# Kernel optimization log

Hardware: AMD Instinct MI355X
Metric: run time of the kernel (lower is better)

## Reference

```python
import jax, jax.numpy as jnp
import numpy as np

MIN_NORM = 1e-15
PROJ_EPS = 4e-3   # HGCN fp32 boundary eps
C = 1.0           # curvature (args.c)
SQRT_C = 1.0
LOOP_ATT = 10.0   # self-loop weight


def _norm(x):
    return jnp.clip(jnp.linalg.norm(x, axis=-1, keepdims=True), MIN_NORM)


def artanh(x):
    x = jnp.clip(x, -1.0 + 1e-6, 1.0 - 1e-6)
    return 0.5 * (jnp.log1p(x) - jnp.log1p(-x))


def proj(x):
    # project back inside the Poincare ball
    n = _norm(x)
    maxn = (1.0 - PROJ_EPS) / SQRT_C
    return jnp.where(n > maxn, x / n * maxn, x)


def expmap0(u):
    n = _norm(u)
    return jnp.tanh(SQRT_C * n) * u / (SQRT_C * n)


def logmap0(p):
    n = _norm(p)
    return artanh(SQRT_C * n) * p / (SQRT_C * n)


def mobius_add(x, y):
    x2 = jnp.sum(x * x, -1, keepdims=True)
    y2 = jnp.sum(y * y, -1, keepdims=True)
    xy = jnp.sum(x * y, -1, keepdims=True)
    num = (1.0 + 2.0 * C * xy + C * y2) * x + (1.0 - C * x2) * y
    den = 1.0 + 2.0 * C * xy + C * C * x2 * y2
    return num / jnp.clip(den, MIN_NORM)


def mobius_matvec(W, x):
    xn = _norm(x)
    mx = x @ W.T                       # [N, out]
    mxn = _norm(mx)
    res = jnp.tanh(mxn / xn * artanh(SQRT_C * xn)) * mx / (mxn * SQRT_C)
    zero = jnp.all(mx == 0, axis=-1, keepdims=True)
    return jnp.where(zero, 0.0, res)


def normalize_adj(adj):
    # symmetric D^{-1/2} A D^{-1/2}
    deg = jnp.sum(adj, axis=-1)
    dinv = jnp.where(deg > 0, deg ** -0.5, 0.0)
    return dinv[:, None] * adj * dinv[None, :]


def encode(x, adj, W_stack, b_stack):
    # map features onto the manifold: proj(expmap0(proj_tan0(x))) ; proj_tan0 = id
    h = proj(expmap0(x))
    for i in range(W_stack.shape[0]):
        # HypLinear: mobius matvec + hyperbolic bias add
        m = proj(mobius_matvec(W_stack[i], h))
        hb = proj(expmap0(b_stack[i][None, :]))
        m = proj(mobius_add(m, hb))
        # HypAgg: aggregate in tangent space at origin
        m = proj(expmap0(adj @ logmap0(m)))
        # HypAct: relu in tangent space
        h = proj(expmap0(jax.nn.relu(logmap0(m))))
    return h


def readout(h):
    # cat(global_avg_pool, global_max_pool) over nodes -> [2*d]
    return jnp.concatenate([jnp.mean(h, axis=0), jnp.max(h, axis=0)])


def setup_inputs() -> dict:
    key = jax.random.key(0)
    ks = jax.random.split(key, 12)
    N, F, D, L = 4096, 128, 128, 2
    x1 = jax.random.normal(ks[0], (1, N, F), jnp.float32)
    x2 = jax.random.normal(ks[1], (1, N, F), jnp.float32)
    adj1 = jax.random.uniform(ks[2], (1, N, N), dtype=jnp.float32)
    adj2 = jax.random.uniform(ks[3], (1, N, N), dtype=jnp.float32)
    dist1 = jax.random.uniform(ks[4], (N, N), dtype=jnp.float32)
    dist2 = jax.random.uniform(ks[5], (N, N), dtype=jnp.float32)
    W_stack = jax.random.normal(ks[6], (L, D, F), jnp.float32) * 0.05
    b_stack = jax.random.normal(ks[7], (L, D), jnp.float32) * 0.01
    W_mlp1 = jax.random.normal(ks[8], (D, 6 * D), jnp.float32) * 0.05
    b_mlp1 = jnp.zeros((D,), jnp.float32)
    W_mlp2 = jax.random.normal(ks[9], (1, D), jnp.float32) * 0.05
    b_mlp2 = jnp.zeros((1,), jnp.float32)
    return dict(x1=x1, x2=x2, adj1=adj1, adj2=adj2, dist1=dist1, dist2=dist2,
                W_stack=W_stack, b_stack=b_stack,
                W_mlp1=W_mlp1, b_mlp1=b_mlp1, W_mlp2=W_mlp2, b_mlp2=b_mlp2)


def reference(x1, x2, adj1, adj2, dist1, dist2, W_stack, b_stack,
              W_mlp1, b_mlp1, W_mlp2, b_mlp2):
    N = x1.shape[1]
    eye = jnp.eye(N, dtype=x1.dtype)
    a1 = normalize_adj(adj1[0] + LOOP_ATT * eye)
    a2 = normalize_adj(adj2[0] + LOOP_ATT * eye)
    out1 = encode(x1[0], a1, W_stack, b_stack)
    out2 = encode(x2[0], a2, W_stack, b_stack)
    h1 = readout(out1)
    h2 = readout(out2)
    feat = jnp.concatenate([h1, h2, h1 - h2])            # [6*d]
    hidden = jax.nn.gelu(feat @ W_mlp1.T + b_mlp1, approximate=False)
    logits = hidden @ W_mlp2.T + b_mlp2                  # [1]
    return logits
```

## Files before the change

kernel.cpp:

```cpp
#include <hip/hip_runtime.h>
#include <math.h>

#define MIN_NORM 1e-15f
#define MAXN 0.996f

typedef __attribute__((ext_vector_type(8))) short bf16x8;
typedef __attribute__((ext_vector_type(16))) float f32x16;

union U8 { unsigned short s[8]; bf16x8 v; };

static __device__ __forceinline__ float wsum(float v) {
#pragma unroll
    for (int o = 32; o > 0; o >>= 1) v += __shfl_xor(v, o, 64);
    return v;
}
static __device__ __forceinline__ float artanh_f(float x) {
    const float lim = 1.0f - 1e-6f;
    x = fminf(fmaxf(x, -lim), lim);
    return 0.5f * (log1pf(x) - log1pf(-x));
}

static __device__ __forceinline__ void split3(float a, unsigned short& h,
                                              unsigned short& l, unsigned short& ll) {
    unsigned u = __float_as_uint(a);
    unsigned hb = u & 0xFFFF0000u;
    float r1 = a - __uint_as_float(hb);
    unsigned u1 = __float_as_uint(r1);
    unsigned lb = u1 & 0xFFFF0000u;
    float r2 = r1 - __uint_as_float(lb);
    unsigned u2 = __float_as_uint(r2);
    unsigned t = u2 + 0x7FFFu + ((u2 >> 16) & 1u);
    h = (unsigned short)(hb >> 16);
    l = (unsigned short)(lb >> 16);
    ll = (unsigned short)(t >> 16);
}

__global__ void k_transW(const float* __restrict__ W, float* __restrict__ Wt) {
    int l = blockIdx.y;
    int t = blockIdx.x * 256 + threadIdx.x;
    int k = t >> 7, d = t & 127;
    Wt[l * 16384 + k * 128 + d] = W[l * 16384 + d * 128 + k];
}

__global__ void k_hb(const float* __restrict__ b_stack, float* __restrict__ hb) {
    int l = blockIdx.x;
    int lane = threadIdx.x;
    float2 b = ((const float2*)(b_stack + l * 128))[lane];
    float n = fmaxf(sqrtf(wsum(b.x * b.x + b.y * b.y)), MIN_NORM);
    float sc = tanhf(n) / n;
    float hx = sc * b.x, hy = sc * b.y;
    float nm = fmaxf(sqrtf(wsum(hx * hx + hy * hy)), MIN_NORM);
    if (nm > MAXN) { float s = MAXN / nm; hx *= s; hy *= s; }
    ((float2*)(hb + l * 128))[lane] = make_float2(hx, hy);
}

__global__ __launch_bounds__(256) void k_deg(const float* __restrict__ adj1,
                                             const float* __restrict__ adj2,
                                             float* __restrict__ dinv) {
    int row = blockIdx.x, g = blockIdx.y;
    const float* adj = (g ? adj2 : adj1) + (size_t)row * 4096;
    float s = 0.f;
    for (int i = threadIdx.x; i < 1024; i += 256) {
        float4 v = ((const float4*)adj)[i];
        s += v.x + v.y + v.z + v.w;
    }
    s = wsum(s);
    __shared__ float ls[4];
    if ((threadIdx.x & 63) == 0) ls[threadIdx.x >> 6] = s;
    __syncthreads();
    if (threadIdx.x == 0) {
        float t = ls[0] + ls[1] + ls[2] + ls[3] + 10.0f;
        dinv[g * 4096 + row] = (t > 0.f) ? (1.0f / sqrtf(t)) : 0.f;
    }
}

__global__ __launch_bounds__(256) void k_manifold(const float* __restrict__ x1,
                                                  const float* __restrict__ x2,
                                                  float* __restrict__ h) {
    int wid = threadIdx.x >> 6, lane = threadIdx.x & 63;
    int row = blockIdx.x * 4 + wid;
    const float* x = (row < 4096 ? x1 : x2 - (size_t)4096 * 128) + (size_t)row * 128;
    float2 v = ((const float2*)x)[lane];
    float n = fmaxf(sqrtf(wsum(v.x * v.x + v.y * v.y)), MIN_NORM);
    float sc = tanhf(n) / n;
    float hx = sc * v.x, hy = sc * v.y;
    float nm = fmaxf(sqrtf(wsum(hx * hx + hy * hy)), MIN_NORM);
    if (nm > MAXN) { float s = MAXN / nm; hx *= s; hy *= s; }
    ((float2*)(h + (size_t)row * 128))[lane] = make_float2(hx, hy);
}

__global__ __launch_bounds__(256) void k_lin(const float* __restrict__ A,
                                             const float* __restrict__ Bt,
                                             float* __restrict__ C) {
    int r0 = blockIdx.x * 64;
    __shared__ float As[32][64];
    __shared__ float Bs[32][128];
    int t = threadIdx.x;
    int tx = t & 15, ty = t >> 4;
    float acc[4][8] = {};
    int ar = t >> 3;
    int ac = (t & 7) * 4;
    for (int kt = 0; kt < 128; kt += 32) {
        const float* Ap = A + (size_t)(r0 + ar) * 128 + kt + ac;
        float4 v0 = *(const float4*)Ap;
        float4 v1 = *(const float4*)(Ap + 32 * 128);
        As[ac + 0][ar] = v0.x; As[ac + 1][ar] = v0.y; As[ac + 2][ar] = v0.z; As[ac + 3][ar] = v0.w;
        As[ac + 0][ar + 32] = v1.x; As[ac + 1][ar + 32] = v1.y; As[ac + 2][ar + 32] = v1.z; As[ac + 3][ar + 32] = v1.w;
#pragma unroll
        for (int i = 0; i < 4; i++) {
            int f = t + 256 * i;
            int kr = f >> 5, c = (f & 31) * 4;
            *(float4*)&Bs[kr][c] = *(const float4*)(Bt + (size_t)(kt + kr) * 128 + c);
        }
        __syncthreads();
#pragma unroll
        for (int k = 0; k < 32; k++) {
            float4 a = *(const float4*)&As[k][ty * 4];
            float4 b0 = *(const float4*)&Bs[k][tx * 4];
            float4 b1 = *(const float4*)&Bs[k][64 + tx * 4];
            float av[4] = {a.x, a.y, a.z, a.w};
            float bv[8] = {b0.x, b0.y, b0.z, b0.w, b1.x, b1.y, b1.z, b1.w};
#pragma unroll
            for (int i = 0; i < 4; i++)
#pragma unroll
                for (int j = 0; j < 8; j++)
                    acc[i][j] = fmaf(av[i], bv[j], acc[i][j]);
        }
        __syncthreads();
    }
#pragma unroll
    for (int i = 0; i < 4; i++) {
        float* Cr = C + (size_t)(r0 + ty * 4 + i) * 128;
        *(float4*)(Cr + tx * 4) = make_float4(acc[i][0], acc[i][1], acc[i][2], acc[i][3]);
        *(float4*)(Cr + 64 + tx * 4) = make_float4(acc[i][4], acc[i][5], acc[i][6], acc[i][7]);
    }
}

__global__ __launch_bounds__(256) void k_postlin(const float* __restrict__ h,
                                                 const float* __restrict__ mx,
                                                 const float* __restrict__ hb,
                                                 const float* __restrict__ dinv,
                                                 float* __restrict__ tp) {
    int wid = threadIdx.x >> 6, lane = threadIdx.x & 63;
    int row = blockIdx.x * 4 + wid;
    float2 hv = ((const float2*)(h + (size_t)row * 128))[lane];
    float2 mv = ((const float2*)(mx + (size_t)row * 128))[lane];
    float xn = fmaxf(sqrtf(wsum(hv.x * hv.x + hv.y * hv.y)), MIN_NORM);
    float mxn = fmaxf(sqrtf(wsum(mv.x * mv.x + mv.y * mv.y)), MIN_NORM);
    float arg = mxn / xn * artanh_f(xn);
    float sc = tanhf(arg) / mxn;
    float rx = sc * mv.x, ry = sc * mv.y;
    float nr = fmaxf(sqrtf(wsum(rx * rx + ry * ry)), MIN_NORM);
    if (nr > MAXN) { float s = MAXN / nr; rx *= s; ry *= s; }
    float2 bv = ((const float2*)hb)[lane];
    float x2 = wsum(rx * rx + ry * ry);
    float y2 = wsum(bv.x * bv.x + bv.y * bv.y);
    float xy = wsum(rx * bv.x + ry * bv.y);
    float cx = 1.0f + 2.0f * xy + y2;
    float cy = 1.0f - x2;
    float den = fmaxf(1.0f + 2.0f * xy + x2 * y2, MIN_NORM);
    float mxo = (cx * rx + cy * bv.x) / den;
    float myo = (cx * ry + cy * bv.y) / den;
    float nm = fmaxf(sqrtf(wsum(mxo * mxo + myo * myo)), MIN_NORM);
    if (nm > MAXN) { float s = MAXN / nm; mxo *= s; myo *= s; }
    float nm2 = fmaxf(sqrtf(wsum(mxo * mxo + myo * myo)), MIN_NORM);
    float lsc = artanh_f(nm2) / nm2;
    float dv = dinv[row];
    ((float2*)(tp + (size_t)row * 128))[lane] =
        make_float2(dv * (lsc * mxo), dv * (lsc * myo));
}

__global__ __launch_bounds__(256) void k_tsplit(const float* __restrict__ tp,
                                                unsigned short* __restrict__ Ph,
                                                unsigned short* __restrict__ Pl,
                                                unsigned short* __restrict__ Pll) {
    __shared__ float L[64][128];
    int g = blockIdx.y;
    int k0 = blockIdx.x * 64;
    const float* T = tp + ((size_t)g * 4096 + k0) * 128;
    int t = threadIdx.x;
#pragma unroll
    for (int i = 0; i < 8; i++) {
        int f = t + 256 * i;
        int r = f >> 5, c4 = f & 31;
        *(float4*)&L[r][c4 * 4] = *(const float4*)(T + (size_t)r * 128 + c4 * 4);
    }
    __syncthreads();
    int c = t & 127, lhi = t >> 7;
    int c31 = c & 31, ct = c >> 5;
#pragma unroll
    for (int q = 0; q < 4; q++) {
        int kb = (k0 >> 4) + q;
        U8 ah, al, al2;
#pragma unroll
        for (int j = 0; j < 8; j++)
            split3(L[q * 16 + lhi * 8 + j][c], ah.s[j], al.s[j], al2.s[j]);
        size_t off = ((((size_t)g * 256 + kb) * 4 + ct) * 64 + lhi * 32 + c31) * 8;
        *(bf16x8*)(Ph + off) = ah.v;
        *(bf16x8*)(Pl + off) = al.v;
        *(bf16x8*)(Pll + off) = al2.v;
    }
}

__global__ __launch_bounds__(256, 2) void k_agg_mfma(
    const float* __restrict__ adj1, const float* __restrict__ adj2,
    const unsigned short* __restrict__ Ph, const unsigned short* __restrict__ Pl,
    const unsigned short* __restrict__ Pll, float* __restrict__ part) {
    __shared__ __align__(16) unsigned short Bs[2][12][512];
    const int w = threadIdx.x >> 6, lane = threadIdx.x & 63;
    const int mt = blockIdx.x, ks = blockIdx.y, g = blockIdx.z;
    const float* __restrict__ A = g ? adj2 : adj1;
    const int l31 = lane & 31, lhi = lane >> 5;
    const float* Ap = A + (size_t)(mt * 128 + w * 32 + l31) * 4096 + ks * 512 + lhi * 8;

    const unsigned short* src[3];
#pragma unroll
    for (int i = 0; i < 3; i++) {
        int c = w * 3 + i;
        const unsigned short* Pb = (c < 4) ? Ph : ((c < 8) ? Pl : Pll);
        src[i] = Pb + ((((size_t)(g * 256 + ks * 32)) * 4 + (c & 3)) * 64 + lane) * 8;
    }

    f32x16 acc[4] = {};
    float4 a0 = *(const float4*)Ap, a1 = *(const float4*)(Ap + 4);

    {
        bf16x8 r0 = *(const bf16x8*)(src[0]);
        bf16x8 r1 = *(const bf16x8*)(src[1]);
        bf16x8 r2 = *(const bf16x8*)(src[2]);
        *(bf16x8*)&Bs[0][w * 3 + 0][lane * 8] = r0;
        *(bf16x8*)&Bs[0][w * 3 + 1][lane * 8] = r1;
        *(bf16x8*)&Bs[0][w * 3 + 2][lane * 8] = r2;
    }
    __syncthreads();

    for (int t = 0; t < 32; t++) {
        const int cur = t & 1;
        const bool more = (t + 1 < 32);
        bf16x8 r0, r1, r2;
        if (more) {
            size_t adv = (size_t)(t + 1) * 2048;
            r0 = *(const bf16x8*)(src[0] + adv);
            r1 = *(const bf16x8*)(src[1] + adv);
            r2 = *(const bf16x8*)(src[2] + adv);
        }
        const float* An = more ? (Ap + 16) : Ap;
        float4 n0 = *(const float4*)An;
        float4 n1 = *(const float4*)(An + 4);
        Ap += 16;
        bf16x8 bh[4], bl[4], bll[4];
#pragma unroll
        for (int ct = 0; ct < 4; ct++) {
            bh[ct]  = *(const bf16x8*)&Bs[cur][ct][lane * 8];
            bl[ct]  = *(const bf16x8*)&Bs[cur][4 + ct][lane * 8];
            bll[ct] = *(const bf16x8*)&Bs[cur][8 + ct][lane * 8];
        }
        U8 ah, al, al2;
        float av[8] = {a0.x, a0.y, a0.z, a0.w, a1.x, a1.y, a1.z, a1.w};
#pragma unroll
        for (int j = 0; j < 8; j++) split3(av[j], ah.s[j], al.s[j], al2.s[j]);
#pragma unroll
        for (int ct = 0; ct < 4; ct++)
            acc[ct] = __builtin_amdgcn_mfma_f32_32x32x16_bf16(ah.v, bh[ct], acc[ct], 0, 0, 0);
#pragma unroll
        for (int ct = 0; ct < 4; ct++)
            acc[ct] = __builtin_amdgcn_mfma_f32_32x32x16_bf16(al.v, bh[ct], acc[ct], 0, 0, 0);
#pragma unroll
        for (int ct = 0; ct < 4; ct++)
            acc[ct] = __builtin_amdgcn_mfma_f32_32x32x16_bf16(ah.v, bl[ct], acc[ct], 0, 0, 0);
#pragma unroll
        for (int ct = 0; ct < 4; ct++)
            acc[ct] = __builtin_amdgcn_mfma_f32_32x32x16_bf16(al.v, bl[ct], acc[ct], 0, 0, 0);
#pragma unroll
        for (int ct = 0; ct < 4; ct++)
            acc[ct] = __builtin_amdgcn_mfma_f32_32x32x16_bf16(ah.v, bll[ct], acc[ct], 0, 0, 0);
#pragma unroll
        for (int ct = 0; ct < 4; ct++)
            acc[ct] = __builtin_amdgcn_mfma_f32_32x32x16_bf16(al2.v, bh[ct], acc[ct], 0, 0, 0);
        if (more) {
            const int nb = cur ^ 1;
            *(bf16x8*)&Bs[nb][w * 3 + 0][lane * 8] = r0;
            *(bf16x8*)&Bs[nb][w * 3 + 1][lane * 8] = r1;
            *(bf16x8*)&Bs[nb][w * 3 + 2][lane * 8] = r2;
        }
        asm volatile("s_waitcnt lgkmcnt(0)" ::: "memory");
        __builtin_amdgcn_sched_barrier(0);
        __builtin_amdgcn_s_barrier();
        a0 = n0; a1 = n1;
    }

    float* P = part + ((size_t)(g * 8 + ks) * 4096) * 128;
    const int rb = mt * 128 + w * 32 + 4 * lhi;
#pragma unroll
    for (int ct = 0; ct < 4; ct++) {
        const int c = ct * 32 + l31;
#pragma unroll
        for (int q = 0; q < 16; q++) {
            int r = rb + (q & 3) + 8 * (q >> 2);
            P[(size_t)r * 128 + c] = acc[ct][q];
        }
    }
}

__global__ __launch_bounds__(256) void k_reduce(const float* __restrict__ part,
                                                const float* __restrict__ tp,
                                                const float* __restrict__ dinv,
                                                float* __restrict__ h) {
    int wid = threadIdx.x >> 6, lane = threadIdx.x & 63;
    int row = blockIdx.x * 4 + wid;
    int g = row >> 12, rr = row & 4095;
    float sx = 0.f, sy = 0.f;
    const float* P = part + ((size_t)(g * 8) * 4096 + rr) * 128;
#pragma unroll
    for (int ks = 0; ks < 8; ks++) {
        float2 v = ((const float2*)(P + (size_t)ks * 4096 * 128))[lane];
        sx += v.x; sy += v.y;
    }
    float2 tv = ((const float2*)(tp + (size_t)row * 128))[lane];
    float d = dinv[row];
    float vx = d * (sx + 10.0f * tv.x);
    float vy = d * (sy + 10.0f * tv.y);
    float n = fmaxf(sqrtf(wsum(vx * vx + vy * vy)), MIN_NORM);
    float e = tanhf(n) / n;
    float px = e * vx, py = e * vy;
    float nm = fmaxf(sqrtf(wsum(px * px + py * py)), MIN_NORM);
    if (nm > MAXN) { float s = MAXN / nm; px *= s; py *= s; }
    float nm2 = fmaxf(sqrtf(wsum(px * px + py * py)), MIN_NORM);
    float lsc = artanh_f(nm2) / nm2;
    float tx2 = fmaxf(lsc * px, 0.0f), ty2 = fmaxf(lsc * py, 0.0f);
    float nr = fmaxf(sqrtf(wsum(tx2 * tx2 + ty2 * ty2)), MIN_NORM);
    float e2 = tanhf(nr) / nr;
    float hx = e2 * tx2, hy = e2 * ty2;
    float nh = fmaxf(sqrtf(wsum(hx * hx + hy * hy)), MIN_NORM);
    if (nh > MAXN) { float s = MAXN / nh; hx *= s; hy *= s; }
    ((float2*)(h + (size_t)row * 128))[lane] = make_float2(hx, hy);
}

__global__ __launch_bounds__(256) void k_red_part(const float* __restrict__ h,
                                                  float* __restrict__ part) {
    int chunk = blockIdx.x;
    int col = threadIdx.x & 127, half = threadIdx.x >> 7;
    float s = 0.f, m = -INFINITY;
    for (int i = 0; i < 64; i++) {
        int r = chunk * 128 + half * 64 + i;
        float v = h[(size_t)r * 128 + col];
        s += v;
        m = fmaxf(m, v);
    }
    __shared__ float ss[128], sm[128];
    if (half) { ss[col] = s; sm[col] = m; }
    __syncthreads();
    if (!half) {
        s += ss[col];
        m = fmaxf(m, sm[col]);
        part[(chunk * 2 + 0) * 128 + col] = s;
        part[(chunk * 2 + 1) * 128 + col] = m;
    }
}

__global__ void k_red_final(const float* __restrict__ part, float* __restrict__ feat) {
    int g = blockIdx.x, col = threadIdx.x;
    float s = 0.f, m = -INFINITY;
    for (int c = g * 32; c < g * 32 + 32; c++) {
        s += part[(c * 2 + 0) * 128 + col];
        m = fmaxf(m, part[(c * 2 + 1) * 128 + col]);
    }
    feat[g * 256 + col] = s * (1.0f / 4096.0f);
    feat[g * 256 + 128 + col] = m;
}

__global__ __launch_bounds__(256) void k_mlp_hidden(const float* __restrict__ feat,
                                                    const float* __restrict__ W1,
                                                    const float* __restrict__ b1,
                                                    float* __restrict__ hidden) {
    int j = blockIdx.x;
    int t = threadIdx.x;
    float p = 0.f;
    for (int k = t; k < 768; k += 256) {
        float f = (k < 512) ? feat[k] : (feat[k - 512] - feat[k - 256]);
        p = fmaf(f, W1[j * 768 + k], p);
    }
    p = wsum(p);
    __shared__ float ps[4];
    if ((t & 63) == 0) ps[t >> 6] = p;
    __syncthreads();
    if (t == 0) {
        float x = ps[0] + ps[1] + ps[2] + ps[3] + b1[j];
        hidden[j] = 0.5f * x * (1.0f + erff(x * 0.70710678118654752f));
    }
}

__global__ void k_mlp_out(const float* __restrict__ hidden, const float* __restrict__ W2,
                          const float* __restrict__ b2, float* __restrict__ out) {
    int t = threadIdx.x;
    float v = hidden[t] * W2[t];
    v = wsum(v);
    __shared__ float ps[2];
    if ((t & 63) == 0) ps[t >> 6] = v;
    __syncthreads();
    if (t == 0) out[0] = ps[0] + ps[1] + b2[0];
}

extern "C" void kernel_launch(void* const* d_in, const int* in_sizes, int n_in,
                              void* d_out, int out_size, void* d_ws, size_t ws_size,
                              hipStream_t stream) {
    (void)in_sizes; (void)n_in; (void)out_size; (void)ws_size;
    const float* x1 = (const float*)d_in[0];
    const float* x2 = (const float*)d_in[1];
    const float* adj1 = (const float*)d_in[2];
    const float* adj2 = (const float*)d_in[3];
    const float* W_stack = (const float*)d_in[6];
    const float* b_stack = (const float*)d_in[7];
    const float* W1 = (const float*)d_in[8];
    const float* b1 = (const float*)d_in[9];
    const float* W2 = (const float*)d_in[10];
    const float* b2 = (const float*)d_in[11];

    float* ws = (float*)d_ws;
    float* dinv = ws;
    float* hb   = ws + 8192;
    float* Wt   = ws + 8448;
    float* h    = ws + 41216;
    float* mx   = h + 1048576;
    float* tp   = mx + 1048576;
    float* part = tp + 1048576;
    float* rpart = part + 8388608;
    float* feat = rpart + 16384;
    float* hid  = feat + 512;
    unsigned short* Ph  = (unsigned short*)(hid + 128);
    unsigned short* Pl  = Ph + 2 * 128 * 4096;
    unsigned short* Pll = Pl + 2 * 128 * 4096;

    k_transW<<<dim3(64, 2), 256, 0, stream>>>(W_stack, Wt);
    k_hb<<<2, 64, 0, stream>>>(b_stack, hb);
    k_deg<<<dim3(4096, 2), 256, 0, stream>>>(adj1, adj2, dinv);
    k_manifold<<<2048, 256, 0, stream>>>(x1, x2, h);
    for (int l = 0; l < 2; l++) {
        k_lin<<<128, 256, 0, stream>>>(h, Wt + l * 16384, mx);
        k_postlin<<<2048, 256, 0, stream>>>(h, mx, hb + l * 128, dinv, tp);
        k_tsplit<<<dim3(64, 2), 256, 0, stream>>>(tp, Ph, Pl, Pll);
        k_agg_mfma<<<dim3(32, 8, 2), 256, 0, stream>>>(adj1, adj2, Ph, Pl, Pll, part);
        k_reduce<<<2048, 256, 0, stream>>>(part, tp, dinv, h);
    }
    k_red_part<<<64, 256, 0, stream>>>(h, rpart);
    k_red_final<<<2, 128, 0, stream>>>(rpart, feat);
    k_mlp_hidden<<<128, 256, 0, stream>>>(feat, W1, b1, hid);
    k_mlp_out<<<1, 128, 0, stream>>>(hid, W2, b2, (float*)d_out);
}
```

Before: 218.1 us.

## Fuse small kernels and double K-step per barrier in MFMA aggregation

Merges the W transpose with the bias expmap kernel, fuses the post-linear manifold math into the bf16 split kernel, and folds the readout finalisation and both MLP layers into one single-block tail kernel. This cuts kernel launches and drops one tp round-trip through global memory. The aggregation MFMA loop now handles two 16-wide K chunks per iteration with a larger LDS buffer, halving barrier count. The fused post-lin kernel launches only 128 blocks instead of 2048, which lowers parallelism for that stage, and the larger LDS footprint may reduce occupancy.

```diff
diff --git a/kernel.cpp b/kernel.cpp
--- a/kernel.cpp
+++ b/kernel.cpp
@@ -35,23 +35,22 @@
     ll = (unsigned short)(t >> 16);
 }
 
-__global__ void k_transW(const float* __restrict__ W, float* __restrict__ Wt) {
+__global__ void k_transW_hb(const float* __restrict__ W, float* __restrict__ Wt,
+                            const float* __restrict__ b_stack, float* __restrict__ hb) {
     int l = blockIdx.y;
     int t = blockIdx.x * 256 + threadIdx.x;
     int k = t >> 7, d = t & 127;
     Wt[l * 16384 + k * 128 + d] = W[l * 16384 + d * 128 + k];
-}
-
-__global__ void k_hb(const float* __restrict__ b_stack, float* __restrict__ hb) {
-    int l = blockIdx.x;
-    int lane = threadIdx.x;
-    float2 b = ((const float2*)(b_stack + l * 128))[lane];
-    float n = fmaxf(sqrtf(wsum(b.x * b.x + b.y * b.y)), MIN_NORM);
-    float sc = tanhf(n) / n;
-    float hx = sc * b.x, hy = sc * b.y;
-    float nm = fmaxf(sqrtf(wsum(hx * hx + hy * hy)), MIN_NORM);
-    if (nm > MAXN) { float s = MAXN / nm; hx *= s; hy *= s; }
-    ((float2*)(hb + l * 128))[lane] = make_float2(hx, hy);
+    if (blockIdx.x == 0 && threadIdx.x < 64) {
+        int lane = threadIdx.x;
+        float2 b = ((const float2*)(b_stack + l * 128))[lane];
+        float n = fmaxf(sqrtf(wsum(b.x * b.x + b.y * b.y)), MIN_NORM);
+        float sc = tanhf(n) / n;
+        float hx = sc * b.x, hy = sc * b.y;
+        float nm = fmaxf(sqrtf(wsum(hx * hx + hy * hy)), MIN_NORM);
+        if (nm > MAXN) { float s = MAXN / nm; hx *= s; hy *= s; }
+        ((float2*)(hb + l * 128))[lane] = make_float2(hx, hy);
+    }
 }
 
 __global__ __launch_bounds__(256) void k_deg(const float* __restrict__ adj1,
@@ -136,56 +135,51 @@
     }
 }
 
-__global__ __launch_bounds__(256) void k_postlin(const float* __restrict__ h,
-                                                 const float* __restrict__ mx,
-                                                 const float* __restrict__ hb,
-                                                 const float* __restrict__ dinv,
-                                                 float* __restrict__ tp) {
-    int wid = threadIdx.x >> 6, lane = threadIdx.x & 63;
-    int row = blockIdx.x * 4 + wid;
-    float2 hv = ((const float2*)(h + (size_t)row * 128))[lane];
-    float2 mv = ((const float2*)(mx + (size_t)row * 128))[lane];
-    float xn = fmaxf(sqrtf(wsum(hv.x * hv.x + hv.y * hv.y)), MIN_NORM);
-    float mxn = fmaxf(sqrtf(wsum(mv.x * mv.x + mv.y * mv.y)), MIN_NORM);
-    float arg = mxn / xn * artanh_f(xn);
-    float sc = tanhf(arg) / mxn;
-    float rx = sc * mv.x, ry = sc * mv.y;
-    float nr = fmaxf(sqrtf(wsum(rx * rx + ry * ry)), MIN_NORM);
-    if (nr > MAXN) { float s = MAXN / nr; rx *= s; ry *= s; }
-    float2 bv = ((const float2*)hb)[lane];
-    float x2 = wsum(rx * rx + ry * ry);
-    float y2 = wsum(bv.x * bv.x + bv.y * bv.y);
-    float xy = wsum(rx * bv.x + ry * bv.y);
-    float cx = 1.0f + 2.0f * xy + y2;
-    float cy = 1.0f - x2;
-    float den = fmaxf(1.0f + 2.0f * xy + x2 * y2, MIN_NORM);
-    float mxo = (cx * rx + cy * bv.x) / den;
-    float myo = (cx * ry + cy * bv.y) / den;
-    float nm = fmaxf(sqrtf(wsum(mxo * mxo + myo * myo)), MIN_NORM);
-    if (nm > MAXN) { float s = MAXN / nm; mxo *= s; myo *= s; }
-    float nm2 = fmaxf(sqrtf(wsum(mxo * mxo + myo * myo)), MIN_NORM);
-    float lsc = artanh_f(nm2) / nm2;
-    float dv = dinv[row];
-    ((float2*)(tp + (size_t)row * 128))[lane] =
-        make_float2(dv * (lsc * mxo), dv * (lsc * myo));
-}
-
-__global__ __launch_bounds__(256) void k_tsplit(const float* __restrict__ tp,
-                                                unsigned short* __restrict__ Ph,
-                                                unsigned short* __restrict__ Pl,
-                                                unsigned short* __restrict__ Pll) {
+__global__ __launch_bounds__(256) void k_posttsplit(const float* __restrict__ h,
+                                                    const float* __restrict__ mx,
+                                                    const float* __restrict__ hb,
+                                                    const float* __restrict__ dinv,
+                                                    float* __restrict__ tp,
+                                                    unsigned short* __restrict__ Ph,
+                                                    unsigned short* __restrict__ Pl,
+                                                    unsigned short* __restrict__ Pll) {
     __shared__ float L[64][128];
     int g = blockIdx.y;
     int k0 = blockIdx.x * 64;
-    const float* T = tp + ((size_t)g * 4096 + k0) * 128;
+    int w = threadIdx.x >> 6, lane = threadIdx.x & 63;
+    for (int q = 0; q < 16; q++) {
+        int r = w * 16 + q;
+        int row = g * 4096 + k0 + r;
+        float2 hv = ((const float2*)(h + (size_t)row * 128))[lane];
+        float2 mv = ((const float2*)(mx + (size_t)row * 128))[lane];
+        float xn = fmaxf(sqrtf(wsum(hv.x * hv.x + hv.y * hv.y)), MIN_NORM);
+        float mxn = fmaxf(sqrtf(wsum(mv.x * mv.x + mv.y * mv.y)), MIN_NORM);
+        float arg = mxn / xn * artanh_f(xn);
+        float sc = tanhf(arg) / mxn;
+        float rx = sc * mv.x, ry = sc * mv.y;
+        float nr = fmaxf(sqrtf(wsum(rx * rx + ry * ry)), MIN_NORM);
+        if (nr > MAXN) { float s = MAXN / nr; rx *= s; ry *= s; }
+        float2 bv = ((const float2*)hb)[lane];
+        float x2 = wsum(rx * rx + ry * ry);
+        float y2 = wsum(bv.x * bv.x + bv.y * bv.y);
+        float xy = wsum(rx * bv.x + ry * bv.y);
+        float cx = 1.0f + 2.0f * xy + y2;
+        float cy = 1.0f - x2;
+        float den = fmaxf(1.0f + 2.0f * xy + x2 * y2, MIN_NORM);
+        float mxo = (cx * rx + cy * bv.x) / den;
+        float myo = (cx * ry + cy * bv.y) / den;
+        float nm = fmaxf(sqrtf(wsum(mxo * mxo + myo * myo)), MIN_NORM);
+        if (nm > MAXN) { float s = MAXN / nm; mxo *= s; myo *= s; }
+        float nm2 = fmaxf(sqrtf(wsum(mxo * mxo + myo * myo)), MIN_NORM);
+        float lsc = artanh_f(nm2) / nm2;
+        float dv = dinv[row];
+        float ox = dv * (lsc * mxo), oy = dv * (lsc * myo);
+        L[r][2 * lane] = ox;
+        L[r][2 * lane + 1] = oy;
+        ((float2*)(tp + (size_t)row * 128))[lane] = make_float2(ox, oy);
+    }
+    __syncthreads();
     int t = threadIdx.x;
-#pragma unroll
-    for (int i = 0; i < 8; i++) {
-        int f = t + 256 * i;
-        int r = f >> 5, c4 = f & 31;
-        *(float4*)&L[r][c4 * 4] = *(const float4*)(T + (size_t)r * 128 + c4 * 4);
-    }
-    __syncthreads();
     int c = t & 127, lhi = t >> 7;
     int c31 = c & 31, ct = c >> 5;
 #pragma unroll
@@ -202,11 +196,45 @@
     }
 }
 
+static __device__ __forceinline__ void step16(const unsigned short Bsc[][512], int cb,
+                                              int lane, float4 a0, float4 a1,
+                                              f32x16* acc) {
+    bf16x8 bh[4], bl[4], bll[4];
+#pragma unroll
+    for (int ct = 0; ct < 4; ct++) {
+        bh[ct]  = *(const bf16x8*)&Bsc[cb + ct][lane * 8];
+        bl[ct]  = *(const bf16x8*)&Bsc[cb + 4 + ct][lane * 8];
+        bll[ct] = *(const bf16x8*)&Bsc[cb + 8 + ct][lane * 8];
+    }
+    U8 ah, al, al2;
+    float av[8] = {a0.x, a0.y, a0.z, a0.w, a1.x, a1.y, a1.z, a1.w};
+#pragma unroll
+    for (int j = 0; j < 8; j++) split3(av[j], ah.s[j], al.s[j], al2.s[j]);
+#pragma unroll
+    for (int ct = 0; ct < 4; ct++)
+        acc[ct] = __builtin_amdgcn_mfma_f32_32x32x16_bf16(ah.v, bh[ct], acc[ct], 0, 0, 0);
+#pragma unroll
+    for (int ct = 0; ct < 4; ct++)
+        acc[ct] = __builtin_amdgcn_mfma_f32_32x32x16_bf16(al.v, bh[ct], acc[ct], 0, 0, 0);
+#pragma unroll
+    for (int ct = 0; ct < 4; ct++)
+        acc[ct] = __builtin_amdgcn_mfma_f32_32x32x16_bf16(ah.v, bl[ct], acc[ct], 0, 0, 0);
+#pragma unroll
+    for (int ct = 0; ct < 4; ct++)
+        acc[ct] = __builtin_amdgcn_mfma_f32_32x32x16_bf16(al.v, bl[ct], acc[ct], 0, 0, 0);
+#pragma unroll
+    for (int ct = 0; ct < 4; ct++)
+        acc[ct] = __builtin_amdgcn_mfma_f32_32x32x16_bf16(ah.v, bll[ct], acc[ct], 0, 0, 0);
+#pragma unroll
+    for (int ct = 0; ct < 4; ct++)
+        acc[ct] = __builtin_amdgcn_mfma_f32_32x32x16_bf16(al2.v, bh[ct], acc[ct], 0, 0, 0);
+}
+
 __global__ __launch_bounds__(256, 2) void k_agg_mfma(
     const float* __restrict__ adj1, const float* __restrict__ adj2,
     const unsigned short* __restrict__ Ph, const unsigned short* __restrict__ Pl,
     const unsigned short* __restrict__ Pll, float* __restrict__ part) {
-    __shared__ __align__(16) unsigned short Bs[2][12][512];
+    __shared__ __align__(16) unsigned short Bs[2][24][512];
     const int w = threadIdx.x >> 6, lane = threadIdx.x & 63;
     const int mt = blockIdx.x, ks = blockIdx.y, g = blockIdx.z;
     const float* __restrict__ A = g ? adj2 : adj1;
@@ -222,71 +250,57 @@
     }
 
     f32x16 acc[4] = {};
-    float4 a0 = *(const float4*)Ap, a1 = *(const float4*)(Ap + 4);
+    float4 a0 = *(const float4*)Ap,        a1 = *(const float4*)(Ap + 4);
+    float4 a2 = *(const float4*)(Ap + 16), a3 = *(const float4*)(Ap + 20);
 
     {
         bf16x8 r0 = *(const bf16x8*)(src[0]);
         bf16x8 r1 = *(const bf16x8*)(src[1]);
         bf16x8 r2 = *(const bf16x8*)(src[2]);
+        bf16x8 r3 = *(const bf16x8*)(src[0] + 2048);
+        bf16x8 r4 = *(const bf16x8*)(src[1] + 2048);
+        bf16x8 r5 = *(const bf16x8*)(src[2] + 2048);
         *(bf16x8*)&Bs[0][w * 3 + 0][lane * 8] = r0;
         *(bf16x8*)&Bs[0][w * 3 + 1][lane * 8] = r1;
         *(bf16x8*)&Bs[0][w * 3 + 2][lane * 8] = r2;
-    }
-    __syncthreads();
-
-    for (int t = 0; t < 32; t++) {
-        const int cur = t & 1;
-        const bool more = (t + 1 < 32);
-        bf16x8 r0, r1, r2;
+        *(bf16x8*)&Bs[0][12 + w * 3 + 0][lane * 8] = r3;
+        *(bf16x8*)&Bs[0][12 + w * 3 + 1][lane * 8] = r4;
+        *(bf16x8*)&Bs[0][12 + w * 3 + 2][lane * 8] = r5;
+    }
+    __syncthreads();
+
+    for (int p = 0; p < 16; p++) {
+        const int cur = p & 1;
+        const bool more = (p + 1 < 16);
+        bf16x8 r0, r1, r2, r3, r4, r5;
         if (more) {
-            size_t adv = (size_t)(t + 1) * 2048;
+            size_t adv = (size_t)(2 * (p + 1)) * 2048;
             r0 = *(const bf16x8*)(src[0] + adv);
             r1 = *(const bf16x8*)(src[1] + adv);
             r2 = *(const bf16x8*)(src[2] + adv);
-        }
-        const float* An = more ? (Ap + 16) : Ap;
-        float4 n0 = *(const float4*)An;
-        float4 n1 = *(const float4*)(An + 4);
-        Ap += 16;
-        bf16x8 bh[4], bl[4], bll[4];
-#pragma unroll
-        for (int ct = 0; ct < 4; ct++) {
-            bh[ct]  = *(const bf16x8*)&Bs[cur][ct][lane * 8];
-            bl[ct]  = *(const bf16x8*)&Bs[cur][4 + ct][lane * 8];
-            bll[ct] = *(const bf16x8*)&Bs[cur][8 + ct][lane * 8];
-        }
-        U8 ah, al, al2;
-        float av[8] = {a0.x, a0.y, a0.z, a0.w, a1.x, a1.y, a1.z, a1.w};
-#pragma unroll
-        for (int j = 0; j < 8; j++) split3(av[j], ah.s[j], al.s[j], al2.s[j]);
-#pragma unroll
-        for (int ct = 0; ct < 4; ct++)
-            acc[ct] = __builtin_amdgcn_mfma_f32_32x32x16_bf16(ah.v, bh[ct], acc[ct], 0, 0, 0);
-#pragma unroll
-        for (int ct = 0; ct < 4; ct++)
-            acc[ct] = __builtin_amdgcn_mfma_f32_32x32x16_bf16(al.v, bh[ct], acc[ct], 0, 0, 0);
-#pragma unroll
-        for (int ct = 0; ct < 4; ct++)
-            acc[ct] = __builtin_amdgcn_mfma_f32_32x32x16_bf16(ah.v, bl[ct], acc[ct], 0, 0, 0);
-#pragma unroll
-        for (int ct = 0; ct < 4; ct++)
-            acc[ct] = __builtin_amdgcn_mfma_f32_32x32x16_bf16(al.v, bl[ct], acc[ct], 0, 0, 0);
-#pragma unroll
-        for (int ct = 0; ct < 4; ct++)
-            acc[ct] = __builtin_amdgcn_mfma_f32_32x32x16_bf16(ah.v, bll[ct], acc[ct], 0, 0, 0);
-#pragma unroll
-        for (int ct = 0; ct < 4; ct++)
-            acc[ct] = __builtin_amdgcn_mfma_f32_32x32x16_bf16(al2.v, bh[ct], acc[ct], 0, 0, 0);
+            r3 = *(const bf16x8*)(src[0] + adv + 2048);
+            r4 = *(const bf16x8*)(src[1] + adv + 2048);
+            r5 = *(const bf16x8*)(src[2] + adv + 2048);
+        }
+        const float* An = more ? (Ap + 32) : Ap;
+        float4 n0 = *(const float4*)An,        n1 = *(const float4*)(An + 4);
+        float4 n2 = *(const float4*)(An + 16), n3 = *(const float4*)(An + 20);
+        Ap += 32;
+        step16(Bs[cur], 0,  lane, a0, a1, acc);
+        step16(Bs[cur], 12, lane, a2, a3, acc);
         if (more) {
             const int nb = cur ^ 1;
             *(bf16x8*)&Bs[nb][w * 3 + 0][lane * 8] = r0;
             *(bf16x8*)&Bs[nb][w * 3 + 1][lane * 8] = r1;
             *(bf16x8*)&Bs[nb][w * 3 + 2][lane * 8] = r2;
+            *(bf16x8*)&Bs[nb][12 + w * 3 + 0][lane * 8] = r3;
+            *(bf16x8*)&Bs[nb][12 + w * 3 + 1][lane * 8] = r4;
+            *(bf16x8*)&Bs[nb][12 + w * 3 + 2][lane * 8] = r5;
         }
         asm volatile("s_waitcnt lgkmcnt(0)" ::: "memory");
         __builtin_amdgcn_sched_barrier(0);
         __builtin_amdgcn_s_barrier();
-        a0 = n0; a1 = n1;
+        a0 = n0; a1 = n1; a2 = n2; a3 = n3;
     }
 
     float* P = part + ((size_t)(g * 8 + ks) * 4096) * 128;
@@ -358,47 +372,46 @@
     }
 }
 
-__global__ void k_red_final(const float* __restrict__ part, float* __restrict__ feat) {
-    int g = blockIdx.x, col = threadIdx.x;
-    float s = 0.f, m = -INFINITY;
-    for (int c = g * 32; c < g * 32 + 32; c++) {
-        s += part[(c * 2 + 0) * 128 + col];
-        m = fmaxf(m, part[(c * 2 + 1) * 128 + col]);
-    }
-    feat[g * 256 + col] = s * (1.0f / 4096.0f);
-    feat[g * 256 + 128 + col] = m;
-}
-
-__global__ __launch_bounds__(256) void k_mlp_hidden(const float* __restrict__ feat,
-                                                    const float* __restrict__ W1,
-                                                    const float* __restrict__ b1,
-                                                    float* __restrict__ hidden) {
-    int j = blockIdx.x;
+__global__ __launch_bounds__(256) void k_tail(const float* __restrict__ rpart,
+                                              const float* __restrict__ W1,
+                                              const float* __restrict__ b1,
+                                              const float* __restrict__ W2,
+                                              const float* __restrict__ b2,
+                                              float* __restrict__ out) {
+    __shared__ float F[512];
+    __shared__ float H[128];
     int t = threadIdx.x;
-    float p = 0.f;
-    for (int k = t; k < 768; k += 256) {
-        float f = (k < 512) ? feat[k] : (feat[k - 512] - feat[k - 256]);
-        p = fmaf(f, W1[j * 768 + k], p);
-    }
-    p = wsum(p);
-    __shared__ float ps[4];
-    if ((t & 63) == 0) ps[t >> 6] = p;
-    __syncthreads();
-    if (t == 0) {
-        float x = ps[0] + ps[1] + ps[2] + ps[3] + b1[j];
-        hidden[j] = 0.5f * x * (1.0f + erff(x * 0.70710678118654752f));
-    }
-}
-
-__global__ void k_mlp_out(const float* __restrict__ hidden, const float* __restrict__ W2,
-                          const float* __restrict__ b2, float* __restrict__ out) {
-    int t = threadIdx.x;
-    float v = hidden[t] * W2[t];
-    v = wsum(v);
-    __shared__ float ps[2];
-    if ((t & 63) == 0) ps[t >> 6] = v;
-    __syncthreads();
-    if (t == 0) out[0] = ps[0] + ps[1] + b2[0];
+    {
+        int g = t >> 7, col = t & 127;
+        float s = 0.f, m = -INFINITY;
+        for (int c = g * 32; c < g * 32 + 32; c++) {
+            s += rpart[(c * 2 + 0) * 128 + col];
+            m = fmaxf(m, rpart[(c * 2 + 1) * 128 + col]);
+        }
+        F[g * 256 + col] = s * (1.0f / 4096.0f);
+        F[g * 256 + 128 + col] = m;
+    }
+    __syncthreads();
+    int w = t >> 6, lane = t & 63;
+    for (int i = 0; i < 32; i++) {
+        int j = w * 32 + i;
+        float p = 0.f;
+        for (int k = lane; k < 768; k += 64) {
+            float f = (k < 512) ? F[k] : (F[k - 512] - F[k - 256]);
+            p = fmaf(f, W1[j * 768 + k], p);
+        }
+        p = wsum(p);
+        if (lane == 0) {
+            float x = p + b1[j];
+            H[j] = 0.5f * x * (1.0f + erff(x * 0.70710678118654752f));
+        }
+    }
+    __syncthreads();
+    if (w == 0) {
+        float v = H[lane] * W2[lane] + H[lane + 64] * W2[lane + 64];
+        v = wsum(v);
+        if (lane == 0) out[0] = v + b2[0];
+    }
 }
 
 extern "C" void kernel_launch(void* const* d_in, const int* in_sizes, int n_in,
@@ -425,25 +438,20 @@
     float* tp   = mx + 1048576;
     float* part = tp + 1048576;
     float* rpart = part + 8388608;
-    float* feat = rpart + 16384;
-    float* hid  = feat + 512;
-    unsigned short* Ph  = (unsigned short*)(hid + 128);
+    unsigned short* Ph  = (unsigned short*)(rpart + 16384);
     unsigned short* Pl  = Ph + 2 * 128 * 4096;
     unsigned short* Pll = Pl + 2 * 128 * 4096;
 
-    k_transW<<<dim3(64, 2), 256, 0, stream>>>(W_stack, Wt);
-    k_hb<<<2, 64, 0, stream>>>(b_stack, hb);
+    k_transW_hb<<<dim3(64, 2), 256, 0, stream>>>(W_stack, Wt, b_stack, hb);
     k_deg<<<dim3(4096, 2), 256, 0, stream>>>(adj1, adj2, dinv);
     k_manifold<<<2048, 256, 0, stream>>>(x1, x2, h);
     for (int l = 0; l < 2; l++) {
         k_lin<<<128, 256, 0, stream>>>(h, Wt + l * 16384, mx);
-        k_postlin<<<2048, 256, 0, stream>>>(h, mx, hb + l * 128, dinv, tp);
-        k_tsplit<<<dim3(64, 2), 256, 0, stream>>>(tp, Ph, Pl, Pll);
+        k_posttsplit<<<dim3(64, 2), 256, 0, stream>>>(h, mx, hb + l * 128, dinv, tp,
+                                                      Ph, Pl, Pll);
         k_agg_mfma<<<dim3(32, 8, 2), 256, 0, stream>>>(adj1, adj2, Ph, Pl, Pll, part);
         k_reduce<<<2048, 256, 0, stream>>>(part, tp, dinv, h);
     }
     k_red_part<<<64, 256, 0, stream>>>(h, rpart);
-    k_red_final<<<2, 128, 0, stream>>>(rpart, feat);
-    k_mlp_hidden<<<128, 256, 0, stream>>>(feat, W1, b1, hid);
-    k_mlp_out<<<1, 128, 0, stream>>>(hid, W2, b2, (float*)d_out);
-}
+    k_tail<<<1, 256, 0, stream>>>(rpart, W1, b1, W2, b2, (float*)d_out);
+}
```

Measured after the change: 381.4 us. +74.9%, slower.
